# Optimization experiments

Measured on AMD Instinct MI355X. Metric: run time of the kernel, lower is better.

Reference implementation:

```python
import jax, jax.numpy as jnp
import numpy as np

TOP_K = 8


def setup_inputs() -> dict:
    key = jax.random.key(0)
    ks = jax.random.split(key, 5)
    T, H, I, E = 4096, 2048, 1024, 64
    s = 0.02
    return {
        "x": jax.random.normal(ks[0], (T, H), jnp.float32),
        "gate_w": jax.random.normal(ks[1], (E, H), jnp.float32) * s,
        "gate_b": jax.random.normal(ks[2], (E,), jnp.float32) * s,
        "fc1_w": jax.random.normal(ks[3], (E, 2 * I, H), jnp.float32) * s,
        "fc2_w": jax.random.normal(ks[4], (E, H, I), jnp.float32) * s,
    }


def reference(x, gate_w, gate_b, fc1_w, fc2_w):
    # Router: [T, E] logits, top-k, softmax over selected logits in fp32.
    E = gate_w.shape[0]
    logits = x @ gate_w.T + gate_b
    topk_logits, topk_idx = jax.lax.top_k(logits, TOP_K)
    w = jax.nn.softmax(topk_logits.astype(jnp.float32), axis=-1).astype(x.dtype)
    # Per-token combine weight for each expert: [T, E] (0 if expert not selected).
    comb = (jax.nn.one_hot(topk_idx, E, dtype=x.dtype) * w[..., None]).sum(axis=1)
    # Scan over experts: each step is one dense GEMM-GeGLU-GEMM with masked combine.
    def body(acc, ew):
        W1, W2, c = ew  # W1 [2I, H], W2 [H, I], c [T]
        h_full = x @ W1.T                       # [T, 2I]
        h, g = jnp.split(h_full, 2, axis=-1)
        a = jax.nn.gelu(h, approximate=False) * (g + 1.0)  # custom GeGLU
        y = a @ W2.T                            # [T, H]
        return acc + c[:, None] * y, None

    out0 = jnp.zeros_like(x)
    out, _ = jax.lax.scan(body, out0, (fc1_w, fc2_w, comb.T))
    return out
```

## Files before the change

### kernel.cpp

```cpp
#include <hip/hip_runtime.h>
#include <hip/hip_bf16.h>
#include <cfloat>
#include <math.h>

#define T_TOK 4096
#define H_DIM 2048
#define E_NUM 64
#define I_DIM 1024
#define TOPK  8
#define BM    256
#define BK    32
#define MAXT  192

typedef __attribute__((ext_vector_type(4))) float f32x4;
typedef __attribute__((ext_vector_type(8))) short bf16x8;
typedef __attribute__((ext_vector_type(4))) int   i32x4;

__device__ __forceinline__ unsigned short f2bf(float f) {
    union { float f; unsigned int u; } v; v.f = f;
    unsigned int r = v.u + 0x7FFFu + ((v.u >> 16) & 1u);
    return (unsigned short)(r >> 16);
}
__device__ __forceinline__ unsigned int pack2(float a, float b) {
    return (unsigned int)f2bf(a) | ((unsigned int)f2bf(b) << 16);
}
__device__ __forceinline__ float bf2f(unsigned short u) {
    union { unsigned int u; float f; } v; v.u = (unsigned int)u << 16; return v.f;
}
__device__ __forceinline__ int cvtpk(float lo, float hi) {
    int r; asm("v_cvt_pk_bf16_f32 %0, %1, %2" : "=v"(r) : "v"(lo), "v"(hi)); return r;
}
__device__ __forceinline__ void gload16(const void* g, void* l) {
    __builtin_amdgcn_global_load_lds((const __attribute__((address_space(1))) unsigned int*)g,
                                     (__attribute__((address_space(3))) unsigned int*)l, 16, 0, 0);
}
__device__ __forceinline__ int xr(int row) { return (row & 3) ^ ((row >> 2) & 3); }

#define WAIT_VM4   do { asm volatile("s_waitcnt vmcnt(4)" ::: "memory"); __builtin_amdgcn_sched_barrier(0); } while(0)
#define WAIT_VM0   do { asm volatile("s_waitcnt vmcnt(0)" ::: "memory"); __builtin_amdgcn_sched_barrier(0); } while(0)
#define WAIT_LGKM0 do { asm volatile("s_waitcnt lgkmcnt(0)" ::: "memory"); __builtin_amdgcn_sched_barrier(0); } while(0)
#define BAR __builtin_amdgcn_s_barrier()

__global__ __launch_bounds__(256)
void router_kernel(const float* __restrict__ x, const float* __restrict__ gw,
                   const float* __restrict__ gb, unsigned short* __restrict__ xb,
                   int* __restrict__ topk_idx, float* __restrict__ topk_w,
                   int* __restrict__ counts)
{
    const int t = blockIdx.x;
    const int tid = threadIdx.x;
    __shared__ float xs[H_DIM];
    __shared__ float logits[E_NUM];
    const float* xrow = x + (size_t)t * H_DIM;

    #pragma unroll
    for (int i = 0; i < 2; ++i) {
        int c = i * 1024 + tid * 4;
        f32x4 v = *(const f32x4*)(xrow + c);
        *(f32x4*)(xs + c) = v;
        uint2 pk; pk.x = pack2(v.x, v.y); pk.y = pack2(v.z, v.w);
        *(uint2*)(xb + (size_t)t * H_DIM + c) = pk;
    }
    __syncthreads();

    const int wave = tid >> 6, lane = tid & 63;
    for (int ee = 0; ee < 16; ++ee) {
        const int e = wave * 16 + ee;
        const float* g = gw + (size_t)e * H_DIM;
        float p = 0.f;
        #pragma unroll
        for (int i = 0; i < 8; ++i) {
            int c = (i * 64 + lane) * 4;
            f32x4 gv = *(const f32x4*)(g + c);
            f32x4 xv = *(const f32x4*)(xs + c);
            p += gv.x * xv.x + gv.y * xv.y + gv.z * xv.z + gv.w * xv.w;
        }
        #pragma unroll
        for (int s = 32; s > 0; s >>= 1) p += __shfl_xor(p, s, 64);
        if (lane == 0) logits[e] = p + gb[e];
    }
    __syncthreads();

    if (tid < 64) {
        float cur = logits[tid];
        float wv[TOPK]; int wi[TOPK];
        #pragma unroll
        for (int k = 0; k < TOPK; ++k) {
            float bv = cur; int bi = tid;
            #pragma unroll
            for (int s = 32; s > 0; s >>= 1) {
                float ov = __shfl_xor(bv, s, 64);
                int   oi = __shfl_xor(bi, s, 64);
                if (ov > bv || (ov == bv && oi < bi)) { bv = ov; bi = oi; }
            }
            wv[k] = bv; wi[k] = bi;
            if (tid == bi) cur = -FLT_MAX;
        }
        if (tid == 0) {
            float mx = wv[0], sum = 0.f, ex[TOPK];
            #pragma unroll
            for (int k = 0; k < TOPK; ++k) { ex[k] = expf(wv[k] - mx); sum += ex[k]; }
            #pragma unroll
            for (int k = 0; k < TOPK; ++k) {
                topk_idx[t * TOPK + k] = wi[k];
                topk_w[t * TOPK + k]   = ex[k] / sum;
                atomicAdd(&counts[wi[k]], 1);
            }
        }
    }
}

__global__ void scan_kernel(const int* __restrict__ counts, int* __restrict__ offsets,
                            int* __restrict__ cursors, int* __restrict__ tiles,
                            int* __restrict__ ntiles)
{
    if (threadIdx.x == 0) {
        int acc = 0, nt = 0;
        for (int e = 0; e < E_NUM; ++e) {
            offsets[e] = acc; cursors[e] = acc;
            int c = counts[e];
            for (int m = 0; m * BM < c; ++m) tiles[nt++] = (e << 16) | m;
            acc += c;
        }
        *ntiles = nt;
    }
}

__global__ void assign_kernel(const int* __restrict__ topk_idx, const float* __restrict__ topk_w,
                              int* __restrict__ cursors, int* __restrict__ tok_of,
                              int* __restrict__ pos_of)
{
    int i = blockIdx.x * 256 + threadIdx.x;
    if (i >= T_TOK * TOPK) return;
    int e = topk_idx[i];
    int pos = atomicAdd(&cursors[e], 1);
    tok_of[pos] = i >> 3;
    pos_of[i]   = pos;
}

__global__ __launch_bounds__(256, 2)
void gemm1_kernel(const unsigned short* __restrict__ xb, const float* __restrict__ fc1,
                  const int* __restrict__ counts, const int* __restrict__ offsets,
                  const int* __restrict__ tok_of, const int* __restrict__ tiles,
                  const int* __restrict__ ntiles, unsigned short* __restrict__ a_all)
{
    const int ty = blockIdx.y;
    if (ty >= *ntiles) return;
    const int code = tiles[ty];
    const int e = code >> 16, m0 = (code & 0xffff) * BM;
    const int cnt = counts[e], off = offsets[e];
    const int pn0 = blockIdx.x * 64;
    const float* W = fc1 + (size_t)e * (size_t)(2 * I_DIM) * H_DIM;

    __shared__ unsigned short sA[2][BM * BK];
    __shared__ unsigned short sB[2][128 * BK];
    __shared__ int sTok[BM];

    const int tid = threadIdx.x;
    sTok[tid] = tok_of[off + ((m0 + tid) < cnt ? (m0 + tid) : cnt - 1)];
    __syncthreads();

    const int wid = tid >> 6, lane = tid & 63;
    const int srow = tid >> 2, sch = tid & 3;
    const int brow = tid >> 1, bhalf = tid & 1;

    const unsigned short* aSrc[4];
    #pragma unroll
    for (int i = 0; i < 4; ++i) {
        int row = srow + 64 * i;
        aSrc[i] = xb + (size_t)sTok[row] * H_DIM + (sch ^ xr(row)) * 8;
    }
    const int wrow = (brow < 64) ? (pn0 + brow) : (I_DIM + pn0 + (brow - 64));
    const float* bSrc = W + (size_t)wrow * H_DIM + bhalf * 16;

    f32x4 accH[8][2], accG[8][2];
    #pragma unroll
    for (int m = 0; m < 8; ++m)
        #pragma unroll
        for (int n = 0; n < 2; ++n) {
            accH[m][n] = (f32x4){0.f, 0.f, 0.f, 0.f};
            accG[m][n] = (f32x4){0.f, 0.f, 0.f, 0.f};
        }

    const int wm = (wid >> 1) * 128;
    const int wnp = (wid & 1) * 32;
    const int fr = lane & 15;
    const int kg = lane >> 4;

    f32x4 br[4];

    auto loadB = [&](int k0) {
        #pragma unroll
        for (int j = 0; j < 4; ++j) br[j] = *(const f32x4*)(bSrc + k0 + j * 4);
    };
    auto issueA = [&](int k0, int buf) {
        #pragma unroll
        for (int i = 0; i < 4; ++i)
            gload16(aSrc[i] + k0, &sA[buf][i * 2048 + tid * 8]);
    };
    auto storeB = [&](int buf) {
        #pragma unroll
        for (int j = 0; j < 2; ++j) {
            i32x4 pk = (i32x4){cvtpk(br[2*j].x,   br[2*j].y),
                               cvtpk(br[2*j].z,   br[2*j].w),
                               cvtpk(br[2*j+1].x, br[2*j+1].y),
                               cvtpk(br[2*j+1].z, br[2*j+1].w)};
            int s = bhalf * 2 + j;
            *(i32x4*)((char*)sB[buf] + brow * 64 + ((s ^ xr(brow)) * 16)) = pk;
        }
    };
    auto compute = [&](int buf) {
        bf16x8 af[8], bh[2], bg[2];
        #pragma unroll
        for (int m = 0; m < 8; ++m) {
            int row = wm + m * 16 + fr;
            af[m] = *(const bf16x8*)((const char*)sA[buf] + row * 64 + ((kg ^ xr(row)) * 16));
        }
        #pragma unroll
        for (int n = 0; n < 2; ++n) {
            int rh = wnp + n * 16 + fr;
            bh[n] = *(const bf16x8*)((const char*)sB[buf] + rh * 64 + ((kg ^ xr(rh)) * 16));
            int rg = 64 + rh;
            bg[n] = *(const bf16x8*)((const char*)sB[buf] + rg * 64 + ((kg ^ xr(rg)) * 16));
        }
        __builtin_amdgcn_s_setprio(1);
        #pragma unroll
        for (int m = 0; m < 8; ++m)
            #pragma unroll
            for (int n = 0; n < 2; ++n) {
                accH[m][n] = __builtin_amdgcn_mfma_f32_16x16x32_bf16(af[m], bh[n], accH[m][n], 0, 0, 0);
                accG[m][n] = __builtin_amdgcn_mfma_f32_16x16x32_bf16(af[m], bg[n], accG[m][n], 0, 0, 0);
            }
        __builtin_amdgcn_s_setprio(0);
    };

    const int NT = H_DIM / BK;
    loadB(0);
    issueA(0, 0);
    WAIT_VM4;
    storeB(0);
    loadB(BK);
    WAIT_VM4;
    WAIT_LGKM0;
    BAR;

    int cur = 0;
    #pragma unroll 1
    for (int t = 0; t < NT; ++t) {
        const bool n1 = (t + 1) < NT, n2 = (t + 2) < NT;
        if (n1) {
            issueA((t + 1) * BK, cur ^ 1);
            WAIT_VM4;
            storeB(cur ^ 1);
        }
        if (n2) loadB((t + 2) * BK);
        compute(cur);
        if (n2)      { WAIT_VM4; }
        else if (n1) { WAIT_VM0; }
        WAIT_LGKM0;
        BAR;
        cur ^= 1;
    }

    #pragma unroll
    for (int m = 0; m < 8; ++m) {
        int rbase = wm + m * 16 + kg * 4;
        #pragma unroll
        for (int r = 0; r < 4; ++r) {
            int gm = m0 + rbase + r;
            if (gm < cnt) {
                size_t rowoff = (size_t)(off + gm) * I_DIM + pn0 + wnp;
                #pragma unroll
                for (int n = 0; n < 2; ++n) {
                    float h = accH[m][n][r];
                    float g = accG[m][n][r];
                    float a = 0.5f * h * (1.f + erff(h * 0.70710678118f)) * (g + 1.f);
                    a_all[rowoff + n * 16 + fr] = f2bf(a);
                }
            }
        }
    }
}

__global__ __launch_bounds__(256, 2)
void gemm2_kernel(const unsigned short* __restrict__ a_all, const float* __restrict__ fc2,
                  const int* __restrict__ counts, const int* __restrict__ offsets,
                  const int* __restrict__ tiles, const int* __restrict__ ntiles,
                  unsigned short* __restrict__ y)
{
    const int ty = blockIdx.y;
    if (ty >= *ntiles) return;
    const int code = tiles[ty];
    const int e = code >> 16, m0 = (code & 0xffff) * BM;
    const int cnt = counts[e], off = offsets[e];
    const int n0 = blockIdx.x * 128;
    const float* W = fc2 + (size_t)e * (size_t)H_DIM * I_DIM;

    __shared__ unsigned short sA[2][BM * BK];
    __shared__ unsigned short sB[2][128 * BK];

    const int tid = threadIdx.x;
    const int wid = tid >> 6, lane = tid & 63;
    const int srow = tid >> 2, sch = tid & 3;
    const int brow = tid >> 1, bhalf = tid & 1;

    const unsigned short* aSrc[4];
    #pragma unroll
    for (int i = 0; i < 4; ++i) {
        int row = srow + 64 * i;
        aSrc[i] = a_all + (size_t)(off + m0 + row) * I_DIM + (sch ^ xr(row)) * 8;
    }
    const float* bSrc = W + (size_t)(n0 + brow) * I_DIM + bhalf * 16;

    f32x4 acc[8][4];
    #pragma unroll
    for (int m = 0; m < 8; ++m)
        #pragma unroll
        for (int n = 0; n < 4; ++n) acc[m][n] = (f32x4){0.f, 0.f, 0.f, 0.f};

    const int wm = (wid >> 1) * 128;
    const int wn = (wid & 1) * 64;
    const int fr = lane & 15;
    const int kg = lane >> 4;

    f32x4 br[4];

    auto loadB = [&](int k0) {
        #pragma unroll
        for (int j = 0; j < 4; ++j) br[j] = *(const f32x4*)(bSrc + k0 + j * 4);
    };
    auto issueA = [&](int k0, int buf) {
        #pragma unroll
        for (int i = 0; i < 4; ++i)
            gload16(aSrc[i] + k0, &sA[buf][i * 2048 + tid * 8]);
    };
    auto storeB = [&](int buf) {
        #pragma unroll
        for (int j = 0; j < 2; ++j) {
            i32x4 pk = (i32x4){cvtpk(br[2*j].x,   br[2*j].y),
                               cvtpk(br[2*j].z,   br[2*j].w),
                               cvtpk(br[2*j+1].x, br[2*j+1].y),
                               cvtpk(br[2*j+1].z, br[2*j+1].w)};
            int s = bhalf * 2 + j;
            *(i32x4*)((char*)sB[buf] + brow * 64 + ((s ^ xr(brow)) * 16)) = pk;
        }
    };
    auto compute = [&](int buf) {
        bf16x8 af[8], bf[4];
        #pragma unroll
        for (int m = 0; m < 8; ++m) {
            int row = wm + m * 16 + fr;
            af[m] = *(const bf16x8*)((const char*)sA[buf] + row * 64 + ((kg ^ xr(row)) * 16));
        }
        #pragma unroll
        for (int n = 0; n < 4; ++n) {
            int row = wn + n * 16 + fr;
            bf[n] = *(const bf16x8*)((const char*)sB[buf] + row * 64 + ((kg ^ xr(row)) * 16));
        }
        __builtin_amdgcn_s_setprio(1);
        #pragma unroll
        for (int m = 0; m < 8; ++m)
            #pragma unroll
            for (int n = 0; n < 4; ++n)
                acc[m][n] = __builtin_amdgcn_mfma_f32_16x16x32_bf16(af[m], bf[n], acc[m][n], 0, 0, 0);
        __builtin_amdgcn_s_setprio(0);
    };

    const int NT = I_DIM / BK;
    loadB(0);
    issueA(0, 0);
    WAIT_VM4;
    storeB(0);
    loadB(BK);
    WAIT_VM4;
    WAIT_LGKM0;
    BAR;

    int cur = 0;
    #pragma unroll 1
    for (int t = 0; t < NT; ++t) {
        const bool n1 = (t + 1) < NT, n2 = (t + 2) < NT;
        if (n1) {
            issueA((t + 1) * BK, cur ^ 1);
            WAIT_VM4;
            storeB(cur ^ 1);
        }
        if (n2) loadB((t + 2) * BK);
        compute(cur);
        if (n2)      { WAIT_VM4; }
        else if (n1) { WAIT_VM0; }
        WAIT_LGKM0;
        BAR;
        cur ^= 1;
    }

    #pragma unroll
    for (int m = 0; m < 8; ++m) {
        int rbase = wm + m * 16 + kg * 4;
        #pragma unroll
        for (int r = 0; r < 4; ++r) {
            int gm = m0 + rbase + r;
            if (gm < cnt) {
                size_t rowoff = (size_t)(off + gm) * H_DIM + n0 + wn;
                #pragma unroll
                for (int n = 0; n < 4; ++n)
                    y[rowoff + n * 16 + fr] = f2bf(acc[m][n][r]);
            }
        }
    }
}

__global__ __launch_bounds__(256)
void combine_kernel(const unsigned short* __restrict__ y, const int* __restrict__ pos_of,
                    const float* __restrict__ topk_w, float* __restrict__ out)
{
    const int t = blockIdx.x;
    const int tid = threadIdx.x;
    __shared__ int   sp[TOPK];
    __shared__ float sw[TOPK];
    if (tid < TOPK) {
        sp[tid] = pos_of[t * TOPK + tid];
        sw[tid] = topk_w[t * TOPK + tid];
    }
    __syncthreads();

    const int c0 = tid * 8;
    float acc[8];
    #pragma unroll
    for (int j = 0; j < 8; ++j) acc[j] = 0.f;
    #pragma unroll
    for (int k = 0; k < TOPK; ++k) {
        const float w = sw[k];
        i32x4 v = *(const i32x4*)(y + (size_t)sp[k] * H_DIM + c0);
        const unsigned short* u = (const unsigned short*)&v;
        #pragma unroll
        for (int j = 0; j < 8; ++j) acc[j] += w * bf2f(u[j]);
    }
    float* orow = out + (size_t)t * H_DIM + c0;
    *(f32x4*)orow       = (f32x4){acc[0], acc[1], acc[2], acc[3]};
    *(f32x4*)(orow + 4) = (f32x4){acc[4], acc[5], acc[6], acc[7]};
}

extern "C" void kernel_launch(void* const* d_in, const int* in_sizes, int n_in,
                              void* d_out, int out_size, void* d_ws, size_t ws_size,
                              hipStream_t stream)
{
    const float* x   = (const float*)d_in[0];
    const float* gw  = (const float*)d_in[1];
    const float* gb  = (const float*)d_in[2];
    const float* fc1 = (const float*)d_in[3];
    const float* fc2 = (const float*)d_in[4];
    float* out = (float*)d_out;

    char* ws = (char*)d_ws;
    size_t o = 0;
    auto alloc = [&](size_t b) { void* p = ws + o; o = (o + b + 255) & ~(size_t)255; return p; };
    unsigned short* xb     = (unsigned short*)alloc((size_t)T_TOK * H_DIM * 2);
    int*            tk_idx = (int*)  alloc((size_t)T_TOK * TOPK * 4);
    float*          tk_w   = (float*)alloc((size_t)T_TOK * TOPK * 4);
    int*            counts = (int*)  alloc(E_NUM * 4);
    int*            offs   = (int*)  alloc(E_NUM * 4);
    int*            curs   = (int*)  alloc(E_NUM * 4);
    int*            tiles  = (int*)  alloc(MAXT * 4);
    int*            ntiles = (int*)  alloc(4);
    int*            tok_of = (int*)  alloc((size_t)T_TOK * TOPK * 4);
    int*            pos_of = (int*)  alloc((size_t)T_TOK * TOPK * 4);
    unsigned short* a_all  = (unsigned short*)alloc((size_t)(T_TOK * TOPK + BM) * I_DIM * 2);
    unsigned short* yb     = (unsigned short*)alloc((size_t)(T_TOK * TOPK + BM) * H_DIM * 2);
    (void)ws_size;

    hipMemsetAsync(counts, 0, E_NUM * 4, stream);

    router_kernel<<<T_TOK, 256, 0, stream>>>(x, gw, gb, xb, tk_idx, tk_w, counts);
    scan_kernel<<<1, 64, 0, stream>>>(counts, offs, curs, tiles, ntiles);
    assign_kernel<<<(T_TOK * TOPK + 255) / 256, 256, 0, stream>>>(tk_idx, tk_w, curs, tok_of, pos_of);
    gemm1_kernel<<<dim3(I_DIM / 64, MAXT), 256, 0, stream>>>(xb, fc1, counts, offs, tok_of,
                                                             tiles, ntiles, a_all);
    gemm2_kernel<<<dim3(H_DIM / 128, MAXT), 256, 0, stream>>>(a_all, fc2, counts, offs,
                                                              tiles, ntiles, yb);
    combine_kernel<<<T_TOK, 256, 0, stream>>>(yb, pos_of, tk_w, out);
}
```

Baseline: 1.130 ms.

## Batch router over 8 tokens per block and split GEMM compute around staging

The router kernel now handles 8 tokens per block, so each gate-weight row is loaded into registers once and reused across 8 tokens instead of being re-read for every token. Grid size drops accordingly, and top-k selection is spread over all four waves. In both grouped GEMM kernels the MFMA work per K-step is split into two halves. The first half runs before the wait on the B global load and its LDS store, and the second half runs after, so the load latency can overlap with matrix math. This costs 64KB of shared memory in the router and fewer router blocks in flight.

Measured after the change: 1.144 ms. About the same (+1.3%).

```diff
diff --git a/kernel.cpp b/kernel.cpp
--- a/kernel.cpp
+++ b/kernel.cpp
@@ -47,46 +47,56 @@
                    int* __restrict__ topk_idx, float* __restrict__ topk_w,
                    int* __restrict__ counts)
 {
-    const int t = blockIdx.x;
+    const int t0 = blockIdx.x * 8;
     const int tid = threadIdx.x;
-    __shared__ float xs[H_DIM];
-    __shared__ float logits[E_NUM];
-    const float* xrow = x + (size_t)t * H_DIM;
-
-    #pragma unroll
-    for (int i = 0; i < 2; ++i) {
-        int c = i * 1024 + tid * 4;
-        f32x4 v = *(const f32x4*)(xrow + c);
-        *(f32x4*)(xs + c) = v;
-        uint2 pk; pk.x = pack2(v.x, v.y); pk.y = pack2(v.z, v.w);
-        *(uint2*)(xb + (size_t)t * H_DIM + c) = pk;
+    __shared__ float xs[8][H_DIM];
+    __shared__ float logits[8][E_NUM];
+
+    #pragma unroll
+    for (int tk = 0; tk < 8; ++tk) {
+        const float* xrow = x + (size_t)(t0 + tk) * H_DIM;
+        #pragma unroll
+        for (int i = 0; i < 2; ++i) {
+            int c = i * 1024 + tid * 4;
+            f32x4 v = *(const f32x4*)(xrow + c);
+            *(f32x4*)(&xs[tk][c]) = v;
+            uint2 pk; pk.x = pack2(v.x, v.y); pk.y = pack2(v.z, v.w);
+            *(uint2*)(xb + (size_t)(t0 + tk) * H_DIM + c) = pk;
+        }
     }
     __syncthreads();
 
     const int wave = tid >> 6, lane = tid & 63;
     for (int ee = 0; ee < 16; ++ee) {
         const int e = wave * 16 + ee;
-        const float* g = gw + (size_t)e * H_DIM;
-        float p = 0.f;
-        #pragma unroll
-        for (int i = 0; i < 8; ++i) {
-            int c = (i * 64 + lane) * 4;
-            f32x4 gv = *(const f32x4*)(g + c);
-            f32x4 xv = *(const f32x4*)(xs + c);
-            p += gv.x * xv.x + gv.y * xv.y + gv.z * xv.z + gv.w * xv.w;
-        }
-        #pragma unroll
-        for (int s = 32; s > 0; s >>= 1) p += __shfl_xor(p, s, 64);
-        if (lane == 0) logits[e] = p + gb[e];
+        const float* g = gw + (size_t)e * H_DIM + lane * 4;
+        f32x4 gv[8];
+        #pragma unroll
+        for (int i = 0; i < 8; ++i) gv[i] = *(const f32x4*)(g + i * 256);
+        #pragma unroll
+        for (int tk = 0; tk < 8; ++tk) {
+            float p = 0.f;
+            #pragma unroll
+            for (int i = 0; i < 8; ++i) {
+                f32x4 xv = *(const f32x4*)(&xs[tk][i * 256 + lane * 4]);
+                p += gv[i].x * xv.x + gv[i].y * xv.y + gv[i].z * xv.z + gv[i].w * xv.w;
+            }
+            #pragma unroll
+            for (int s = 32; s > 0; s >>= 1) p += __shfl_xor(p, s, 64);
+            if (lane == 0) logits[tk][e] = p + gb[e];
+        }
     }
     __syncthreads();
 
-    if (tid < 64) {
-        float cur = logits[tid];
+    #pragma unroll
+    for (int j = 0; j < 2; ++j) {
+        const int tk = wave * 2 + j;
+        const int t = t0 + tk;
+        float cur = logits[tk][lane];
         float wv[TOPK]; int wi[TOPK];
         #pragma unroll
         for (int k = 0; k < TOPK; ++k) {
-            float bv = cur; int bi = tid;
+            float bv = cur; int bi = lane;
             #pragma unroll
             for (int s = 32; s > 0; s >>= 1) {
                 float ov = __shfl_xor(bv, s, 64);
@@ -94,9 +104,9 @@
                 if (ov > bv || (ov == bv && oi < bi)) { bv = ov; bi = oi; }
             }
             wv[k] = bv; wi[k] = bi;
-            if (tid == bi) cur = -FLT_MAX;
-        }
-        if (tid == 0) {
+            if (lane == bi) cur = -FLT_MAX;
+        }
+        if (lane == 0) {
             float mx = wv[0], sum = 0.f, ex[TOPK];
             #pragma unroll
             for (int k = 0; k < TOPK; ++k) { ex[k] = expf(wv[k] - mx); sum += ex[k]; }
@@ -209,11 +219,11 @@
             *(i32x4*)((char*)sB[buf] + brow * 64 + ((s ^ xr(brow)) * 16)) = pk;
         }
     };
-    auto compute = [&](int buf) {
-        bf16x8 af[8], bh[2], bg[2];
-        #pragma unroll
-        for (int m = 0; m < 8; ++m) {
-            int row = wm + m * 16 + fr;
+    auto computeHalf = [&](int buf, int mbase) {
+        bf16x8 af[4], bh[2], bg[2];
+        #pragma unroll
+        for (int m = 0; m < 4; ++m) {
+            int row = wm + (mbase + m) * 16 + fr;
             af[m] = *(const bf16x8*)((const char*)sA[buf] + row * 64 + ((kg ^ xr(row)) * 16));
         }
         #pragma unroll
@@ -225,11 +235,11 @@
         }
         __builtin_amdgcn_s_setprio(1);
         #pragma unroll
-        for (int m = 0; m < 8; ++m)
+        for (int m = 0; m < 4; ++m)
             #pragma unroll
             for (int n = 0; n < 2; ++n) {
-                accH[m][n] = __builtin_amdgcn_mfma_f32_16x16x32_bf16(af[m], bh[n], accH[m][n], 0, 0, 0);
-                accG[m][n] = __builtin_amdgcn_mfma_f32_16x16x32_bf16(af[m], bg[n], accG[m][n], 0, 0, 0);
+                accH[mbase + m][n] = __builtin_amdgcn_mfma_f32_16x16x32_bf16(af[m], bh[n], accH[mbase + m][n], 0, 0, 0);
+                accG[mbase + m][n] = __builtin_amdgcn_mfma_f32_16x16x32_bf16(af[m], bg[n], accG[mbase + m][n], 0, 0, 0);
             }
         __builtin_amdgcn_s_setprio(0);
     };
@@ -248,13 +258,14 @@
     #pragma unroll 1
     for (int t = 0; t < NT; ++t) {
         const bool n1 = (t + 1) < NT, n2 = (t + 2) < NT;
+        if (n1) issueA((t + 1) * BK, cur ^ 1);
+        computeHalf(cur, 0);
         if (n1) {
-            issueA((t + 1) * BK, cur ^ 1);
             WAIT_VM4;
             storeB(cur ^ 1);
         }
         if (n2) loadB((t + 2) * BK);
-        compute(cur);
+        computeHalf(cur, 4);
         if (n2)      { WAIT_VM4; }
         else if (n1) { WAIT_VM0; }
         WAIT_LGKM0;
@@ -345,11 +356,11 @@
             *(i32x4*)((char*)sB[buf] + brow * 64 + ((s ^ xr(brow)) * 16)) = pk;
         }
     };
-    auto compute = [&](int buf) {
-        bf16x8 af[8], bf[4];
-        #pragma unroll
-        for (int m = 0; m < 8; ++m) {
-            int row = wm + m * 16 + fr;
+    auto computeHalf = [&](int buf, int mbase) {
+        bf16x8 af[4], bf[4];
+        #pragma unroll
+        for (int m = 0; m < 4; ++m) {
+            int row = wm + (mbase + m) * 16 + fr;
             af[m] = *(const bf16x8*)((const char*)sA[buf] + row * 64 + ((kg ^ xr(row)) * 16));
         }
         #pragma unroll
@@ -359,10 +370,10 @@
         }
         __builtin_amdgcn_s_setprio(1);
         #pragma unroll
-        for (int m = 0; m < 8; ++m)
+        for (int m = 0; m < 4; ++m)
             #pragma unroll
             for (int n = 0; n < 4; ++n)
-                acc[m][n] = __builtin_amdgcn_mfma_f32_16x16x32_bf16(af[m], bf[n], acc[m][n], 0, 0, 0);
+                acc[mbase + m][n] = __builtin_amdgcn_mfma_f32_16x16x32_bf16(af[m], bf[n], acc[mbase + m][n], 0, 0, 0);
         __builtin_amdgcn_s_setprio(0);
     };
 
@@ -380,13 +391,14 @@
     #pragma unroll 1
     for (int t = 0; t < NT; ++t) {
         const bool n1 = (t + 1) < NT, n2 = (t + 2) < NT;
+        if (n1) issueA((t + 1) * BK, cur ^ 1);
+        computeHalf(cur, 0);
         if (n1) {
-            issueA((t + 1) * BK, cur ^ 1);
             WAIT_VM4;
             storeB(cur ^ 1);
         }
         if (n2) loadB((t + 2) * BK);
-        compute(cur);
+        computeHalf(cur, 4);
         if (n2)      { WAIT_VM4; }
         else if (n1) { WAIT_VM0; }
         WAIT_LGKM0;
@@ -471,7 +483,7 @@
 
     hipMemsetAsync(counts, 0, E_NUM * 4, stream);
 
-    router_kernel<<<T_TOK, 256, 0, stream>>>(x, gw, gb, xb, tk_idx, tk_w, counts);
+    router_kernel<<<T_TOK / 8, 256, 0, stream>>>(x, gw, gb, xb, tk_idx, tk_w, counts);
     scan_kernel<<<1, 64, 0, stream>>>(counts, offs, curs, tiles, ntiles);
     assign_kernel<<<(T_TOK * TOPK + 255) / 256, 256, 0, stream>>>(tk_idx, tk_w, curs, tok_of, pos_of);
     gemm1_kernel<<<dim3(I_DIM / 64, MAXT), 256, 0, stream>>>(xb, fc1, counts, offs, tok_of,
```

## Deepen B-operand register prefetch to two tiles ahead in both expert GEMMs

Applied to the files above, without the earlier changes.

Both expert GEMM kernels now keep two register buffers (P and Q) of fp32 weight data, so global loads for B are issued two k-tiles ahead instead of one. The main loop is unrolled by two, alternating the buffers, and ends in an explicit epilogue. This gives weight loads more time to land before they are converted and stored to LDS, which targets memory-latency stalls, in exchange for 16 more VGPRs per thread and more complex vmcnt accounting.

New measurement: 1.140 ms. No clear change (+0.9%).

```diff
diff --git a/kernel.cpp b/kernel.cpp
--- a/kernel.cpp
+++ b/kernel.cpp
@@ -187,24 +187,39 @@
     const int fr = lane & 15;
     const int kg = lane >> 4;
 
-    f32x4 br[4];
-
-    auto loadB = [&](int k0) {
-        #pragma unroll
-        for (int j = 0; j < 4; ++j) br[j] = *(const f32x4*)(bSrc + k0 + j * 4);
+    f32x4 brP[4], brQ[4];
+
+    auto loadP = [&](int k0) {
+        #pragma unroll
+        for (int j = 0; j < 4; ++j) brP[j] = *(const f32x4*)(bSrc + k0 + j * 4);
+    };
+    auto loadQ = [&](int k0) {
+        #pragma unroll
+        for (int j = 0; j < 4; ++j) brQ[j] = *(const f32x4*)(bSrc + k0 + j * 4);
     };
     auto issueA = [&](int k0, int buf) {
         #pragma unroll
         for (int i = 0; i < 4; ++i)
             gload16(aSrc[i] + k0, &sA[buf][i * 2048 + tid * 8]);
     };
-    auto storeB = [&](int buf) {
+    auto storeP = [&](int buf) {
         #pragma unroll
         for (int j = 0; j < 2; ++j) {
-            i32x4 pk = (i32x4){cvtpk(br[2*j].x,   br[2*j].y),
-                               cvtpk(br[2*j].z,   br[2*j].w),
-                               cvtpk(br[2*j+1].x, br[2*j+1].y),
-                               cvtpk(br[2*j+1].z, br[2*j+1].w)};
+            i32x4 pk = (i32x4){cvtpk(brP[2*j].x,   brP[2*j].y),
+                               cvtpk(brP[2*j].z,   brP[2*j].w),
+                               cvtpk(brP[2*j+1].x, brP[2*j+1].y),
+                               cvtpk(brP[2*j+1].z, brP[2*j+1].w)};
+            int s = bhalf * 2 + j;
+            *(i32x4*)((char*)sB[buf] + brow * 64 + ((s ^ xr(brow)) * 16)) = pk;
+        }
+    };
+    auto storeQ = [&](int buf) {
+        #pragma unroll
+        for (int j = 0; j < 2; ++j) {
+            i32x4 pk = (i32x4){cvtpk(brQ[2*j].x,   brQ[2*j].y),
+                               cvtpk(brQ[2*j].z,   brQ[2*j].w),
+                               cvtpk(brQ[2*j+1].x, brQ[2*j+1].y),
+                               cvtpk(brQ[2*j+1].z, brQ[2*j+1].w)};
             int s = bhalf * 2 + j;
             *(i32x4*)((char*)sB[buf] + brow * 64 + ((s ^ xr(brow)) * 16)) = pk;
         }
@@ -235,31 +250,56 @@
     };
 
     const int NT = H_DIM / BK;
-    loadB(0);
+    loadP(0);
     issueA(0, 0);
     WAIT_VM4;
-    storeB(0);
-    loadB(BK);
+    storeP(0);
+    loadP(BK);
+    WAIT_VM4;
+    loadQ(2 * BK);
     WAIT_VM4;
     WAIT_LGKM0;
     BAR;
 
     int cur = 0;
     #pragma unroll 1
-    for (int t = 0; t < NT; ++t) {
-        const bool n1 = (t + 1) < NT, n2 = (t + 2) < NT;
-        if (n1) {
-            issueA((t + 1) * BK, cur ^ 1);
-            WAIT_VM4;
-            storeB(cur ^ 1);
-        }
-        if (n2) loadB((t + 2) * BK);
-        compute(cur);
-        if (n2)      { WAIT_VM4; }
-        else if (n1) { WAIT_VM0; }
+    for (int t = 0; t < NT - 4; t += 2) {
+        storeP(cur ^ 1);
+        issueA((t + 1) * BK, cur ^ 1);
+        loadP((t + 3) * BK);
+        compute(cur);
+        WAIT_VM4;
         WAIT_LGKM0;
         BAR;
         cur ^= 1;
+        storeQ(cur ^ 1);
+        issueA((t + 2) * BK, cur ^ 1);
+        loadQ((t + 4) * BK);
+        compute(cur);
+        WAIT_VM4;
+        WAIT_LGKM0;
+        BAR;
+        cur ^= 1;
+    }
+    {
+        const int t = NT - 4;
+        storeP(cur ^ 1);
+        issueA((t + 1) * BK, cur ^ 1);
+        loadP((t + 3) * BK);
+        compute(cur);
+        WAIT_VM4;
+        WAIT_LGKM0; BAR; cur ^= 1;
+        storeQ(cur ^ 1);
+        issueA((NT - 2) * BK, cur ^ 1);
+        compute(cur);
+        WAIT_VM0;
+        WAIT_LGKM0; BAR; cur ^= 1;
+        storeP(cur ^ 1);
+        issueA((NT - 1) * BK, cur ^ 1);
+        compute(cur);
+        WAIT_VM0;
+        WAIT_LGKM0; BAR; cur ^= 1;
+        compute(cur);
     }
 
     #pragma unroll
@@ -323,24 +363,39 @@
     const int fr = lane & 15;
     const int kg = lane >> 4;
 
-    f32x4 br[4];
-
-    auto loadB = [&](int k0) {
-        #pragma unroll
-        for (int j = 0; j < 4; ++j) br[j] = *(const f32x4*)(bSrc + k0 + j * 4);
+    f32x4 brP[4], brQ[4];
+
+    auto loadP = [&](int k0) {
+        #pragma unroll
+        for (int j = 0; j < 4; ++j) brP[j] = *(const f32x4*)(bSrc + k0 + j * 4);
+    };
+    auto loadQ = [&](int k0) {
+        #pragma unroll
+        for (int j = 0; j < 4; ++j) brQ[j] = *(const f32x4*)(bSrc + k0 + j * 4);
     };
     auto issueA = [&](int k0, int buf) {
         #pragma unroll
         for (int i = 0; i < 4; ++i)
             gload16(aSrc[i] + k0, &sA[buf][i * 2048 + tid * 8]);
     };
-    auto storeB = [&](int buf) {
+    auto storeP = [&](int buf) {
         #pragma unroll
         for (int j = 0; j < 2; ++j) {
-            i32x4 pk = (i32x4){cvtpk(br[2*j].x,   br[2*j].y),
-                               cvtpk(br[2*j].z,   br[2*j].w),
-                               cvtpk(br[2*j+1].x, br[2*j+1].y),
-                               cvtpk(br[2*j+1].z, br[2*j+1].w)};
+            i32x4 pk = (i32x4){cvtpk(brP[2*j].x,   brP[2*j].y),
+                               cvtpk(brP[2*j].z,   brP[2*j].w),
+                               cvtpk(brP[2*j+1].x, brP[2*j+1].y),
+                               cvtpk(brP[2*j+1].z, brP[2*j+1].w)};
+            int s = bhalf * 2 + j;
+            *(i32x4*)((char*)sB[buf] + brow * 64 + ((s ^ xr(brow)) * 16)) = pk;
+        }
+    };
+    auto storeQ = [&](int buf) {
+        #pragma unroll
+        for (int j = 0; j < 2; ++j) {
+            i32x4 pk = (i32x4){cvtpk(brQ[2*j].x,   brQ[2*j].y),
+                               cvtpk(brQ[2*j].z,   brQ[2*j].w),
+                               cvtpk(brQ[2*j+1].x, brQ[2*j+1].y),
+                               cvtpk(brQ[2*j+1].z, brQ[2*j+1].w)};
             int s = bhalf * 2 + j;
             *(i32x4*)((char*)sB[buf] + brow * 64 + ((s ^ xr(brow)) * 16)) = pk;
         }
@@ -367,31 +422,56 @@
     };
 
     const int NT = I_DIM / BK;
-    loadB(0);
+    loadP(0);
     issueA(0, 0);
     WAIT_VM4;
-    storeB(0);
-    loadB(BK);
+    storeP(0);
+    loadP(BK);
+    WAIT_VM4;
+    loadQ(2 * BK);
     WAIT_VM4;
     WAIT_LGKM0;
     BAR;
 
     int cur = 0;
     #pragma unroll 1
-    for (int t = 0; t < NT; ++t) {
-        const bool n1 = (t + 1) < NT, n2 = (t + 2) < NT;
-        if (n1) {
-            issueA((t + 1) * BK, cur ^ 1);
-            WAIT_VM4;
-            storeB(cur ^ 1);
-        }
-        if (n2) loadB((t + 2) * BK);
-        compute(cur);
-        if (n2)      { WAIT_VM4; }
-        else if (n1) { WAIT_VM0; }
+    for (int t = 0; t < NT - 4; t += 2) {
+        storeP(cur ^ 1);
+        issueA((t + 1) * BK, cur ^ 1);
+        loadP((t + 3) * BK);
+        compute(cur);
+        WAIT_VM4;
         WAIT_LGKM0;
         BAR;
         cur ^= 1;
+        storeQ(cur ^ 1);
+        issueA((t + 2) * BK, cur ^ 1);
+        loadQ((t + 4) * BK);
+        compute(cur);
+        WAIT_VM4;
+        WAIT_LGKM0;
+        BAR;
+        cur ^= 1;
+    }
+    {
+        const int t = NT - 4;
+        storeP(cur ^ 1);
+        issueA((t + 1) * BK, cur ^ 1);
+        loadP((t + 3) * BK);
+        compute(cur);
+        WAIT_VM4;
+        WAIT_LGKM0; BAR; cur ^= 1;
+        storeQ(cur ^ 1);
+        issueA((NT - 2) * BK, cur ^ 1);
+        compute(cur);
+        WAIT_VM0;
+        WAIT_LGKM0; BAR; cur ^= 1;
+        storeP(cur ^ 1);
+        issueA((NT - 1) * BK, cur ^ 1);
+        compute(cur);
+        WAIT_VM0;
+        WAIT_LGKM0; BAR; cur ^= 1;
+        compute(cur);
     }
 
     #pragma unroll
```
